# Performance work log

Measured on AMD Instinct MI355X. Metric: run time of the kernel, lower is better.

The kernel has to match this reference:

```python
import jax, jax.numpy as jnp
import numpy as np

CHUNK = 64  # chunk_size from init


def _fused_chunk_fwd(q, k, v, scale, chunk):
    # q,k,v: [B,S,H,D]
    B, S, H, D = q.shape
    NT = S // chunk
    # -> [NT, B, H, chunk, D] for scan over chunks
    def to_chunks(x):
        return x.reshape(B, NT, chunk, H, D).transpose(1, 0, 3, 2, 4)
    qc, kc, vc = to_chunks(q), to_chunks(k), to_chunks(v)
    mask = jnp.tril(jnp.ones((chunk, chunk), dtype=q.dtype))  # row >= col (inclusive)

    def step(h, xs):
        qi, ki, vi = xs  # each [B,H,chunk,D]
        qs = qi * scale
        # intra-chunk causal attention scores (no softmax: linear attention)
        s = jnp.einsum('bhqd,bhkd->bhqk', qs, ki) * mask
        # intra-chunk contribution + inter-chunk recurrent state contribution
        o = jnp.einsum('bhqk,bhke->bhqe', s, vi) + jnp.einsum('bhqd,bhde->bhqe', qs, h)
        # state update: h += K^T V  (strictly after producing this chunk's output)
        h = h + jnp.einsum('bhcd,bhce->bhde', ki, vi)
        return h, o

    h0 = jnp.zeros((B, H, D, D), dtype=jnp.float32)
    hf, oc = jax.lax.scan(step, h0, (qc, kc, vc))
    # oc: [NT,B,H,chunk,D] -> [B,S,H,D]
    o = oc.transpose(1, 0, 3, 2, 4).reshape(B, S, H, D)
    return o, hf


def setup_inputs() -> dict:
    key = jax.random.key(0)
    kq, kk, kv = jax.random.split(key, 3)
    B, S, H, D = 2, 4096, 16, 128
    q = jax.random.normal(kq, (B, S, H, D), dtype=jnp.float32)
    k = jax.random.normal(kk, (B, S, H, D), dtype=jnp.float32)
    v = jax.random.normal(kv, (B, S, H, D), dtype=jnp.float32)
    return {"q": q, "k": k, "v": v}


def reference(q, k, v):
    D = q.shape[-1]
    scale = D ** (-0.5)
    o, final_state = _fused_chunk_fwd(q, k, v, scale, CHUNK)
    return o, final_state
```

## Files before the change

### kernel.cpp

```cpp
#include <hip/hip_runtime.h>
#include <hip/hip_bf16.h>
#include <math.h>

#define BB 2
#define SS 4096
#define HH 16
#define DD 128
#define CK 64
#define NTC 64
#define HD 2048
#define SQ 136
#define ST 72

typedef __attribute__((ext_vector_type(8))) short bh8;
typedef __attribute__((ext_vector_type(16))) float fx16;

#define MFMA32(a, b, c) __builtin_amdgcn_mfma_f32_32x32x16_bf16(a, b, c, 0, 0, 0)
#define SWZ(off, row) ((off) ^ (8 * (((row) >> 3) & 3)))

__device__ inline unsigned pk2(float a, float b) {
    union { __hip_bfloat162 h2; unsigned u; } r;
    r.h2.x = __float2bfloat16(a);
    r.h2.y = __float2bfloat16(b);
    return r.u;
}
#define UPK(u, x, y) { x = __uint_as_float((unsigned)(u) << 16); y = __uint_as_float((unsigned)(u) & 0xFFFF0000u); }

#define SWAP32(x, y) asm("v_permlane32_swap_b32 %0, %1" : "+v"(x), "+v"(y))

#define MKFRAG(dst, cc, O) { \
    unsigned a0_ = pk2(cc[(O)+0], cc[(O)+1]), a1_ = pk2(cc[(O)+2], cc[(O)+3]); \
    unsigned a2_ = pk2(cc[(O)+4], cc[(O)+5]), a3_ = pk2(cc[(O)+6], cc[(O)+7]); \
    SWAP32(a0_, a2_); SWAP32(a1_, a3_); \
    union { unsigned u[4]; bh8 v; } r_; \
    r_.u[0] = a0_; r_.u[1] = a1_; r_.u[2] = a2_; r_.u[3] = a3_; \
    dst = r_.v; }

__global__ __launch_bounds__(512, 2) void ksum_kernel(const float* __restrict__ k,
                                                      const float* __restrict__ v,
                                                      unsigned* __restrict__ G,
                                                      int CPG, int NG) {
    int g = blockIdx.x, h = blockIdx.y, b = blockIdx.z;
    int t = threadIdx.x, l = t & 63, w = t >> 6, hi = l >> 5, lm = l & 31;
    int dbp = 2 * (w >> 2), eb = w & 3;
    __shared__ short lkT[2][128 * ST];
    __shared__ short lvT[2][128 * ST];
    fx16 h0 = {}, h1 = {};
    long hbase = ((long)b * SS) * HD + (long)h * DD;
    float kt[16], vt[16];

#define KLOAD(cc) { long base_ = hbase + (long)(g * CPG + (cc)) * CK * HD; \
    _Pragma("unroll") for (int i = 0; i < 8; ++i) { int it = t + 512 * i; \
        int e = (it & 31) + 32 * (it >> 10); int c2 = (it >> 5) & 31; \
        long ga = base_ + (long)(2 * c2) * HD + e; \
        kt[2*i] = k[ga]; kt[2*i+1] = k[ga + HD]; \
        vt[2*i] = v[ga]; vt[2*i+1] = v[ga + HD]; } }

#define KSTAGE(pn) { \
    _Pragma("unroll") for (int i = 0; i < 8; ++i) { int it = t + 512 * i; \
        int e = (it & 31) + 32 * (it >> 10); int c2 = (it >> 5) & 31; \
        *(unsigned*)&lkT[pn][e * ST + SWZ(2 * c2, e)] = pk2(kt[2*i], kt[2*i+1]); \
        *(unsigned*)&lvT[pn][e * ST + SWZ(2 * c2, e)] = pk2(vt[2*i], vt[2*i+1]); } }

    KLOAD(0); KSTAGE(0); if (CPG > 1) KLOAD(1);
    __syncthreads();
    int p = 0;
    for (int c = 0; c < CPG; ++c) {
        if (c + 1 < CPG) KSTAGE(p ^ 1);
        if (c + 2 < CPG) KLOAD(c + 2);
        bh8 Bv0 = *(const bh8*)&lvT[p][(32*eb+lm)*ST + SWZ( 0 + 8*hi, lm)];
        bh8 Bv1 = *(const bh8*)&lvT[p][(32*eb+lm)*ST + SWZ(16 + 8*hi, lm)];
        bh8 Bv2 = *(const bh8*)&lvT[p][(32*eb+lm)*ST + SWZ(32 + 8*hi, lm)];
        bh8 Bv3 = *(const bh8*)&lvT[p][(32*eb+lm)*ST + SWZ(48 + 8*hi, lm)];
        __builtin_amdgcn_s_setprio(1);
#define KM4(hx, db) { \
        bh8 A0_ = *(const bh8*)&lkT[p][(32*(db)+lm)*ST + SWZ( 0 + 8*hi, lm)]; hx = MFMA32(A0_, Bv0, hx); \
        bh8 A1_ = *(const bh8*)&lkT[p][(32*(db)+lm)*ST + SWZ(16 + 8*hi, lm)]; hx = MFMA32(A1_, Bv1, hx); \
        bh8 A2_ = *(const bh8*)&lkT[p][(32*(db)+lm)*ST + SWZ(32 + 8*hi, lm)]; hx = MFMA32(A2_, Bv2, hx); \
        bh8 A3_ = *(const bh8*)&lkT[p][(32*(db)+lm)*ST + SWZ(48 + 8*hi, lm)]; hx = MFMA32(A3_, Bv3, hx); }
        KM4(h0, dbp) KM4(h1, dbp + 1)
        __builtin_amdgcn_s_setprio(0);
        __syncthreads();
        p ^= 1;
    }
    unsigned* Gp = G + ((long)(b * HH + h) * NG + g) * (DD * DD / 2);
    long t0 = (long)(dbp * 4 + eb) * 512 + l * 8;
    long t1 = (long)((dbp + 1) * 4 + eb) * 512 + l * 8;
    uint4 u;
    u.x = pk2(h0[0],h0[1]);  u.y = pk2(h0[2],h0[3]);  u.z = pk2(h0[4],h0[5]);  u.w = pk2(h0[6],h0[7]);
    *(uint4*)(Gp + t0) = u;
    u.x = pk2(h0[8],h0[9]);  u.y = pk2(h0[10],h0[11]); u.z = pk2(h0[12],h0[13]); u.w = pk2(h0[14],h0[15]);
    *(uint4*)(Gp + t0 + 4) = u;
    u.x = pk2(h1[0],h1[1]);  u.y = pk2(h1[2],h1[3]);  u.z = pk2(h1[4],h1[5]);  u.w = pk2(h1[6],h1[7]);
    *(uint4*)(Gp + t1) = u;
    u.x = pk2(h1[8],h1[9]);  u.y = pk2(h1[10],h1[11]); u.z = pk2(h1[12],h1[13]); u.w = pk2(h1[14],h1[15]);
    *(uint4*)(Gp + t1 + 4) = u;
}

__global__ __launch_bounds__(256) void prefix_kernel(unsigned* __restrict__ G,
                                                     float* __restrict__ hf,
                                                     int NG) {
    int tid = blockIdx.x * 256 + threadIdx.x;
    int bh = tid >> 11;
    int fl = (tid & 2047) * 8;
    unsigned* Gb = G + (long)bh * NG * (DD * DD / 2) + fl / 2;
    float a[8] = {0.f, 0.f, 0.f, 0.f, 0.f, 0.f, 0.f, 0.f};
    uint4 nxt = *(uint4*)Gb;
    for (int g = 0; g < NG; ++g) {
        uint4 cur = nxt;
        if (g + 1 < NG) nxt = *(uint4*)(Gb + (long)(g + 1) * (DD * DD / 2));
        uint4 st;
        st.x = pk2(a[0], a[1]); st.y = pk2(a[2], a[3]);
        st.z = pk2(a[4], a[5]); st.w = pk2(a[6], a[7]);
        *(uint4*)(Gb + (long)g * (DD * DD / 2)) = st;
        float x, y;
        UPK(cur.x, x, y); a[0] += x; a[1] += y;
        UPK(cur.y, x, y); a[2] += x; a[3] += y;
        UPK(cur.z, x, y); a[4] += x; a[5] += y;
        UPK(cur.w, x, y); a[6] += x; a[7] += y;
    }
    float* hb = hf + (long)bh * (DD * DD);
    int tile = fl >> 10, li = (fl >> 4) & 63;
#pragma unroll
    for (int j = 0; j < 8; ++j) {
        int rg = (fl & 15) + j;
        int d = 32 * (tile >> 2) + (rg & 3) + 8 * (rg >> 2) + 4 * (li >> 5);
        int e = 32 * (tile & 3) + (li & 31);
        hb[d * DD + e] = a[j];
    }
}

__global__ __launch_bounds__(512, 2) void scan_kernel(const float* __restrict__ q,
                                                      const float* __restrict__ kk,
                                                      const float* __restrict__ vv,
                                                      const unsigned* __restrict__ G,
                                                      float* __restrict__ o,
                                                      int CPG, int NG, float scale) {
    int g = blockIdx.x, h = blockIdx.y, b = blockIdx.z;
    int t = threadIdx.x, l = t & 63, w = t >> 6, hi = l >> 5, lm = l & 31;
    int rb = w >> 2, eb = w & 3;
    __shared__ short lq [64 * SQ];
    __shared__ short lk [64 * SQ];
    __shared__ short lkT[128 * ST];
    __shared__ short lvT[128 * ST];

    fx16 h0 = {}, h1 = {}, h2 = {}, h3 = {};
    {
        const unsigned* Gp = G + ((long)(b * HH + h) * NG + g) * (DD * DD / 2);
#define GINIT(hx, db) { const unsigned* p_ = Gp + (long)((db) * 4 + eb) * 512 + l * 8; \
        uint4 u0 = *(const uint4*)p_; uint4 u1 = *(const uint4*)(p_ + 4); \
        UPK(u0.x, hx[0], hx[1]);  UPK(u0.y, hx[2], hx[3]); \
        UPK(u0.z, hx[4], hx[5]);  UPK(u0.w, hx[6], hx[7]); \
        UPK(u1.x, hx[8], hx[9]);  UPK(u1.y, hx[10], hx[11]); \
        UPK(u1.z, hx[12], hx[13]); UPK(u1.w, hx[14], hx[15]); }
        GINIT(h0, 0) GINIT(h1, 1) GINIT(h2, 2) GINIT(h3, 3)
    }

    long hbase = ((long)b * SS) * HD + (long)h * DD;
    int r8 = t >> 3, c8 = t & 7;

    for (int c = 0; c < CPG; ++c) {
        long base = hbase + (long)(g * CPG + c) * CK * HD;
#pragma unroll
        for (int j = 0; j < 4; ++j) {
            long ga = base + (long)r8 * HD + 4 * c8 + 32 * j;
            float4 qv = *(const float4*)&q[ga];
            float4 kv = *(const float4*)&kk[ga];
            uint2 uq; uq.x = pk2(qv.x * scale, qv.y * scale); uq.y = pk2(qv.z * scale, qv.w * scale);
            *(uint2*)&lq[r8 * SQ + SWZ(4 * c8 + 32 * j, r8)] = uq;
            uint2 uk; uk.x = pk2(kv.x, kv.y); uk.y = pk2(kv.z, kv.w);
            *(uint2*)&lk[r8 * SQ + SWZ(4 * c8 + 32 * j, r8)] = uk;
        }
#pragma unroll
        for (int i = 0; i < 8; ++i) {
            int it = t + 512 * i;
            int e = (it & 31) + 32 * (it >> 10);
            int c2 = (it >> 5) & 31;
            long ga = base + (long)(2 * c2) * HD + e;
            *(unsigned*)&lkT[e * ST + SWZ(2 * c2, e)] = pk2(kk[ga], kk[ga + HD]);
            *(unsigned*)&lvT[e * ST + SWZ(2 * c2, e)] = pk2(vv[ga], vv[ga + HD]);
        }
        __syncthreads();

        __builtin_amdgcn_s_setprio(1);
        fx16 sa = {};
#pragma unroll
        for (int ks = 0; ks < 8; ++ks) {
            bh8 Bq = *(const bh8*)&lq[(32*rb+lm)*SQ + SWZ(16*ks + 8*hi, lm)];
            bh8 A0 = *(const bh8*)&lk[lm*SQ + SWZ(16*ks + 8*hi, lm)];
            sa = MFMA32(A0, Bq, sa);
        }
        bh8 fS0, fS1, fS2, fS3;
        if (rb == 0) {
            float ms[16];
#pragma unroll
            for (int rg = 0; rg < 16; ++rg) {
                int cc_ = (rg & 3) + 8 * (rg >> 2) + 4 * hi;
                ms[rg] = (cc_ <= lm) ? sa[rg] : 0.f;
            }
            MKFRAG(fS0, ms, 0) MKFRAG(fS1, ms, 8)
        } else {
            MKFRAG(fS0, sa, 0) MKFRAG(fS1, sa, 8)
            fx16 sb = {};
#pragma unroll
            for (int ks = 0; ks < 8; ++ks) {
                bh8 Bq = *(const bh8*)&lq[(32+lm)*SQ + SWZ(16*ks + 8*hi, lm)];
                bh8 A1 = *(const bh8*)&lk[(32+lm)*SQ + SWZ(16*ks + 8*hi, lm)];
                sb = MFMA32(A1, Bq, sb);
            }
            float ms[16];
#pragma unroll
            for (int rg = 0; rg < 16; ++rg) {
                int cc_ = 32 + (rg & 3) + 8 * (rg >> 2) + 4 * hi;
                ms[rg] = (cc_ <= 32 + lm) ? sb[rg] : 0.f;
            }
            MKFRAG(fS2, ms, 0) MKFRAG(fS3, ms, 8)
        }

        bh8 Bv0 = *(const bh8*)&lvT[(32*eb+lm)*ST + SWZ( 0 + 8*hi, lm)];
        bh8 Bv1 = *(const bh8*)&lvT[(32*eb+lm)*ST + SWZ(16 + 8*hi, lm)];
        bh8 Bv2 = *(const bh8*)&lvT[(32*eb+lm)*ST + SWZ(32 + 8*hi, lm)];
        bh8 Bv3 = *(const bh8*)&lvT[(32*eb+lm)*ST + SWZ(48 + 8*hi, lm)];

        fx16 oa = {};
        oa = MFMA32(fS0, Bv0, oa);
        oa = MFMA32(fS1, Bv1, oa);
        if (rb) {
            oa = MFMA32(fS2, Bv2, oa);
            oa = MFMA32(fS3, Bv3, oa);
        }
#define M3STEP(hx, db) { \
        bh8 Aq0 = *(const bh8*)&lq[(32*rb+lm)*SQ + SWZ(16*(2*(db)) + 8*hi, lm)]; \
        bh8 Bh0; MKFRAG(Bh0, hx, 0); oa = MFMA32(Aq0, Bh0, oa); \
        bh8 Aq1 = *(const bh8*)&lq[(32*rb+lm)*SQ + SWZ(16*(2*(db)+1) + 8*hi, lm)]; \
        bh8 Bh1; MKFRAG(Bh1, hx, 8); oa = MFMA32(Aq1, Bh1, oa); }
        M3STEP(h0, 0) M3STEP(h1, 1) M3STEP(h2, 2) M3STEP(h3, 3)

#define M4STEP(hx, db) { \
        bh8 A0_ = *(const bh8*)&lkT[(32*(db)+lm)*ST + SWZ( 0 + 8*hi, lm)]; hx = MFMA32(A0_, Bv0, hx); \
        bh8 A1_ = *(const bh8*)&lkT[(32*(db)+lm)*ST + SWZ(16 + 8*hi, lm)]; hx = MFMA32(A1_, Bv1, hx); \
        bh8 A2_ = *(const bh8*)&lkT[(32*(db)+lm)*ST + SWZ(32 + 8*hi, lm)]; hx = MFMA32(A2_, Bv2, hx); \
        bh8 A3_ = *(const bh8*)&lkT[(32*(db)+lm)*ST + SWZ(48 + 8*hi, lm)]; hx = MFMA32(A3_, Bv3, hx); }
        M4STEP(h0, 0) M4STEP(h1, 1) M4STEP(h2, 2) M4STEP(h3, 3)
        __builtin_amdgcn_s_setprio(0);

        {
            float* op = o + base;
            int e = 32 * eb + lm;
#pragma unroll
            for (int rg = 0; rg < 16; ++rg) {
                int r = 32 * rb + (rg & 3) + 8 * (rg >> 2) + 4 * hi;
                op[(long)r * HD + e] = oa[rg];
            }
        }
        __syncthreads();
    }
}

extern "C" void kernel_launch(void* const* d_in, const int* in_sizes, int n_in,
                              void* d_out, int out_size, void* d_ws, size_t ws_size,
                              hipStream_t stream) {
    const float* q = (const float*)d_in[0];
    const float* k = (const float*)d_in[1];
    const float* v = (const float*)d_in[2];
    float* o  = (float*)d_out;
    float* hf = o + (long)BB * SS * HH * DD;
    unsigned* G = (unsigned*)d_ws;

    int NG = 16;
    while (NG > 1 && (size_t)BB * HH * NG * DD * DD * 2 > ws_size) NG >>= 1;
    int CPG = NTC / NG;
    float scale = 1.0f / sqrtf((float)DD);

    ksum_kernel<<<dim3(NG, HH, BB), 512, 0, stream>>>(k, v, G, CPG, NG);
    prefix_kernel<<<dim3(256, 1, 1), 256, 0, stream>>>(G, hf, NG);
    scan_kernel<<<dim3(NG, HH, BB), 512, 0, stream>>>(q, k, v, G, o, CPG, NG, scale);
}
```

Measured before the change: 102.8 us.

## Halve scan_kernel block to 4 waves, each computing both row halves

Reduces scan_kernel from 8 to 4 waves per block, with each wave owning one 32-column slice of the output and computing both 32-row halves. Previously 8 waves each handled one row half, so the state update h += K^T V was computed redundantly by the two row-half waves. This change removes that duplicate work and shares the score tiles. The cost is fewer waves available to hide latency, more accumulator registers per wave, and twice as many global load iterations per thread.

```diff
diff --git a/kernel.cpp b/kernel.cpp
--- a/kernel.cpp
+++ b/kernel.cpp
@@ -130,7 +130,7 @@
     }
 }
 
-__global__ __launch_bounds__(512, 2) void scan_kernel(const float* __restrict__ q,
+__global__ __launch_bounds__(256, 2) void scan_kernel(const float* __restrict__ q,
                                                       const float* __restrict__ kk,
                                                       const float* __restrict__ vv,
                                                       const unsigned* __restrict__ G,
@@ -138,7 +138,7 @@
                                                       int CPG, int NG, float scale) {
     int g = blockIdx.x, h = blockIdx.y, b = blockIdx.z;
     int t = threadIdx.x, l = t & 63, w = t >> 6, hi = l >> 5, lm = l & 31;
-    int rb = w >> 2, eb = w & 3;
+    int eb = w;
     __shared__ short lq [64 * SQ];
     __shared__ short lk [64 * SQ];
     __shared__ short lkT[128 * ST];
@@ -157,23 +157,23 @@
     }
 
     long hbase = ((long)b * SS) * HD + (long)h * DD;
-    int r8 = t >> 3, c8 = t & 7;
+    int r4 = t >> 2, c4 = t & 3;
 
     for (int c = 0; c < CPG; ++c) {
         long base = hbase + (long)(g * CPG + c) * CK * HD;
 #pragma unroll
-        for (int j = 0; j < 4; ++j) {
-            long ga = base + (long)r8 * HD + 4 * c8 + 32 * j;
+        for (int j = 0; j < 8; ++j) {
+            long ga = base + (long)r4 * HD + 4 * (c4 + 4 * j);
             float4 qv = *(const float4*)&q[ga];
             float4 kv = *(const float4*)&kk[ga];
             uint2 uq; uq.x = pk2(qv.x * scale, qv.y * scale); uq.y = pk2(qv.z * scale, qv.w * scale);
-            *(uint2*)&lq[r8 * SQ + SWZ(4 * c8 + 32 * j, r8)] = uq;
+            *(uint2*)&lq[r4 * SQ + SWZ(4 * (c4 + 4 * j), r4)] = uq;
             uint2 uk; uk.x = pk2(kv.x, kv.y); uk.y = pk2(kv.z, kv.w);
-            *(uint2*)&lk[r8 * SQ + SWZ(4 * c8 + 32 * j, r8)] = uk;
-        }
-#pragma unroll
-        for (int i = 0; i < 8; ++i) {
-            int it = t + 512 * i;
+            *(uint2*)&lk[r4 * SQ + SWZ(4 * (c4 + 4 * j), r4)] = uk;
+        }
+#pragma unroll
+        for (int i = 0; i < 16; ++i) {
+            int it = t + 256 * i;
             int e = (it & 31) + 32 * (it >> 10);
             int c2 = (it >> 5) & 31;
             long ga = base + (long)(2 * c2) * HD + e;
@@ -183,38 +183,16 @@
         __syncthreads();
 
         __builtin_amdgcn_s_setprio(1);
-        fx16 sa = {};
+        fx16 st00 = {}, st01 = {}, st11 = {};
 #pragma unroll
         for (int ks = 0; ks < 8; ++ks) {
-            bh8 Bq = *(const bh8*)&lq[(32*rb+lm)*SQ + SWZ(16*ks + 8*hi, lm)];
-            bh8 A0 = *(const bh8*)&lk[lm*SQ + SWZ(16*ks + 8*hi, lm)];
-            sa = MFMA32(A0, Bq, sa);
-        }
-        bh8 fS0, fS1, fS2, fS3;
-        if (rb == 0) {
-            float ms[16];
-#pragma unroll
-            for (int rg = 0; rg < 16; ++rg) {
-                int cc_ = (rg & 3) + 8 * (rg >> 2) + 4 * hi;
-                ms[rg] = (cc_ <= lm) ? sa[rg] : 0.f;
-            }
-            MKFRAG(fS0, ms, 0) MKFRAG(fS1, ms, 8)
-        } else {
-            MKFRAG(fS0, sa, 0) MKFRAG(fS1, sa, 8)
-            fx16 sb = {};
-#pragma unroll
-            for (int ks = 0; ks < 8; ++ks) {
-                bh8 Bq = *(const bh8*)&lq[(32+lm)*SQ + SWZ(16*ks + 8*hi, lm)];
-                bh8 A1 = *(const bh8*)&lk[(32+lm)*SQ + SWZ(16*ks + 8*hi, lm)];
-                sb = MFMA32(A1, Bq, sb);
-            }
-            float ms[16];
-#pragma unroll
-            for (int rg = 0; rg < 16; ++rg) {
-                int cc_ = 32 + (rg & 3) + 8 * (rg >> 2) + 4 * hi;
-                ms[rg] = (cc_ <= 32 + lm) ? sb[rg] : 0.f;
-            }
-            MKFRAG(fS2, ms, 0) MKFRAG(fS3, ms, 8)
+            bh8 ak0 = *(const bh8*)&lk[lm * SQ        + SWZ(16*ks + 8*hi, lm)];
+            bh8 ak1 = *(const bh8*)&lk[(32+lm) * SQ   + SWZ(16*ks + 8*hi, lm)];
+            bh8 qf0 = *(const bh8*)&lq[lm * SQ        + SWZ(16*ks + 8*hi, lm)];
+            bh8 qf1 = *(const bh8*)&lq[(32+lm) * SQ   + SWZ(16*ks + 8*hi, lm)];
+            st00 = MFMA32(ak0, qf0, st00);
+            st01 = MFMA32(ak0, qf1, st01);
+            st11 = MFMA32(ak1, qf1, st11);
         }
 
         bh8 Bv0 = *(const bh8*)&lvT[(32*eb+lm)*ST + SWZ( 0 + 8*hi, lm)];
@@ -222,18 +200,41 @@
         bh8 Bv2 = *(const bh8*)&lvT[(32*eb+lm)*ST + SWZ(32 + 8*hi, lm)];
         bh8 Bv3 = *(const bh8*)&lvT[(32*eb+lm)*ST + SWZ(48 + 8*hi, lm)];
 
-        fx16 oa = {};
-        oa = MFMA32(fS0, Bv0, oa);
-        oa = MFMA32(fS1, Bv1, oa);
-        if (rb) {
-            oa = MFMA32(fS2, Bv2, oa);
-            oa = MFMA32(fS3, Bv3, oa);
+        fx16 oa0 = {}, oa1 = {};
+        {
+            float ms[16];
+#pragma unroll
+            for (int rg = 0; rg < 16; ++rg) {
+                int cc_ = (rg & 3) + 8 * (rg >> 2) + 4 * hi;
+                ms[rg] = (cc_ <= lm) ? st00[rg] : 0.f;
+            }
+            bh8 f0, f1; MKFRAG(f0, ms, 0) MKFRAG(f1, ms, 8)
+            oa0 = MFMA32(f0, Bv0, oa0);
+            oa0 = MFMA32(f1, Bv1, oa0);
+        }
+        {
+            bh8 f0, f1; MKFRAG(f0, st01, 0) MKFRAG(f1, st01, 8)
+            oa1 = MFMA32(f0, Bv0, oa1);
+            oa1 = MFMA32(f1, Bv1, oa1);
+            float ms[16];
+#pragma unroll
+            for (int rg = 0; rg < 16; ++rg) {
+                int cc_ = (rg & 3) + 8 * (rg >> 2) + 4 * hi;
+                ms[rg] = (cc_ <= lm) ? st11[rg] : 0.f;
+            }
+            bh8 f2, f3; MKFRAG(f2, ms, 0) MKFRAG(f3, ms, 8)
+            oa1 = MFMA32(f2, Bv2, oa1);
+            oa1 = MFMA32(f3, Bv3, oa1);
         }
 #define M3STEP(hx, db) { \
-        bh8 Aq0 = *(const bh8*)&lq[(32*rb+lm)*SQ + SWZ(16*(2*(db)) + 8*hi, lm)]; \
-        bh8 Bh0; MKFRAG(Bh0, hx, 0); oa = MFMA32(Aq0, Bh0, oa); \
-        bh8 Aq1 = *(const bh8*)&lq[(32*rb+lm)*SQ + SWZ(16*(2*(db)+1) + 8*hi, lm)]; \
-        bh8 Bh1; MKFRAG(Bh1, hx, 8); oa = MFMA32(Aq1, Bh1, oa); }
+        bh8 Bh0; MKFRAG(Bh0, hx, 0); \
+        bh8 Aq0 = *(const bh8*)&lq[lm * SQ      + SWZ(16*(2*(db)) + 8*hi, lm)]; \
+        bh8 Aq1 = *(const bh8*)&lq[(32+lm) * SQ + SWZ(16*(2*(db)) + 8*hi, lm)]; \
+        oa0 = MFMA32(Aq0, Bh0, oa0); oa1 = MFMA32(Aq1, Bh0, oa1); \
+        bh8 Bh1; MKFRAG(Bh1, hx, 8); \
+        bh8 Aq2 = *(const bh8*)&lq[lm * SQ      + SWZ(16*(2*(db)+1) + 8*hi, lm)]; \
+        bh8 Aq3 = *(const bh8*)&lq[(32+lm) * SQ + SWZ(16*(2*(db)+1) + 8*hi, lm)]; \
+        oa0 = MFMA32(Aq2, Bh1, oa0); oa1 = MFMA32(Aq3, Bh1, oa1); }
         M3STEP(h0, 0) M3STEP(h1, 1) M3STEP(h2, 2) M3STEP(h3, 3)
 
 #define M4STEP(hx, db) { \
@@ -249,8 +250,9 @@
             int e = 32 * eb + lm;
 #pragma unroll
             for (int rg = 0; rg < 16; ++rg) {
-                int r = 32 * rb + (rg & 3) + 8 * (rg >> 2) + 4 * hi;
-                op[(long)r * HD + e] = oa[rg];
+                int r = (rg & 3) + 8 * (rg >> 2) + 4 * hi;
+                op[(long)r * HD + e]        = oa0[rg];
+                op[(long)(32 + r) * HD + e] = oa1[rg];
             }
         }
         __syncthreads();
@@ -274,5 +276,5 @@
 
     ksum_kernel<<<dim3(NG, HH, BB), 512, 0, stream>>>(k, v, G, CPG, NG);
     prefix_kernel<<<dim3(256, 1, 1), 256, 0, stream>>>(G, hf, NG);
-    scan_kernel<<<dim3(NG, HH, BB), 512, 0, stream>>>(q, k, v, G, o, CPG, NG, scale);
-}
+    scan_kernel<<<dim3(NG, HH, BB), 256, 0, stream>>>(q, k, v, G, o, CPG, NG, scale);
+}
```

Result: slower. 206.9 us (+101.1%).
